# Kernel optimization log

Hardware: AMD Instinct MI355X
Metric: run time of the kernel (lower is better)

The kernel has to match this reference:

```python
import jax, jax.numpy as jnp
import numpy as np

B, S, H = 1, 2048, 1024
NH, NKV, HD = 16, 4, 64  # n_attn_heads, n_kv_heads, head_dim


def setup_inputs() -> dict:
    key = jax.random.key(0)
    k1, k2, k3, k4 = jax.random.split(key, 4)
    x = jax.random.normal(k1, (B, S, H), dtype=jnp.float32)
    Wq = jax.random.normal(k2, (H, H), dtype=jnp.float32) * 0.02
    Wk = jax.random.normal(k3, (NKV * HD, H), dtype=jnp.float32) * 0.02
    Wv = jax.random.normal(k4, (NKV * HD, H), dtype=jnp.float32) * 0.02
    return {"x": x, "Wq": Wq, "Wk": Wk, "Wv": Wv}


def reference(x, Wq, Wk, Wv):
    b, s, h = x.shape
    rep = NH // NKV
    # projections (torch Linear: x @ W.T)
    q = (x @ Wq.T).reshape(b, s, NH, HD).transpose(0, 2, 1, 3)      # [b, NH, s, d]
    k = (x @ Wk.T).reshape(b, s, NKV, HD).transpose(0, 2, 1, 3)     # [b, NKV, s, d]
    v = (x @ Wv.T).reshape(b, s, NKV, HD).transpose(0, 2, 1, 3)
    # repeat_kv: expand each kv head rep times
    k = jnp.repeat(k, rep, axis=1)                                   # [b, NH, s, d]
    v = jnp.repeat(v, rep, axis=1)
    # NOTE: source scales by 1/sqrt(hidden_size), not 1/sqrt(head_dim)
    scale = 1.0 / np.sqrt(H).astype(np.float32)
    scores = jnp.einsum('bhqd,bhkd->bhqk', q, k) * scale             # [b, NH, s, s]
    causal = jnp.tril(jnp.ones((s, s), dtype=bool))
    scores = jnp.where(causal[None, None], scores, -jnp.inf)
    probs = jax.nn.softmax(scores, axis=-1)
    y = jnp.einsum('bhqk,bhkd->bhqd', probs, v)                      # [b, NH, s, d]
    return y.transpose(0, 2, 1, 3).reshape(b, s, NH * HD)
```

## Files before the change

kernel.cpp:

```cpp
#include <hip/hip_runtime.h>

#define S_LEN 2048
#define HID   1024
#define NHEAD 16
#define NKVH  4
#define HDIM  64
#define NPROJ 1536
#define QKSTR 1280

typedef __bf16 bf16x8 __attribute__((ext_vector_type(8)));
typedef float  f32x4  __attribute__((ext_vector_type(4)));

typedef const __attribute__((address_space(1))) void* gas_ptr;
typedef __attribute__((address_space(3))) void*       las_ptr;

#define QSCALE 0.04508422f

__device__ __forceinline__ unsigned short f2bf(float f) {
    unsigned u = __builtin_bit_cast(unsigned, f);
    u = u + 0x7FFFu + ((u >> 16) & 1u);
    return (unsigned short)(u >> 16);
}

__global__ __launch_bounds__(256) void cvt_all(
    const float* __restrict__ x,  const float* __restrict__ wq,
    const float* __restrict__ wk, const float* __restrict__ wv,
    unsigned short* __restrict__ xbf, unsigned short* __restrict__ wbf)
{
    const long nx  = (long)S_LEN * HID;
    const long nwq = (long)HID * HID;
    const long nwk = (long)256 * HID;
    long i = (long)(blockIdx.x * 256 + threadIdx.x) * 4;
    const float* src; unsigned short* dst;
    if (i < nx)                  { src = x  + i;                 dst = xbf + i; }
    else if (i < nx + nwq)       { long j = i - nx;              src = wq + j; dst = wbf + j; }
    else if (i < nx + nwq + nwk) { long j = i - nx - nwq;        src = wk + j; dst = wbf + nwq + j; }
    else                         { long j = i - nx - nwq - nwk;  src = wv + j; dst = wbf + nwq + nwk + j; }
    float4 v = *(const float4*)src;
    ushort4 o; o.x = f2bf(v.x); o.y = f2bf(v.y); o.z = f2bf(v.z); o.w = f2bf(v.w);
    *(ushort4*)dst = o;
}

__global__ __launch_bounds__(256) void proj_gemm(
    const unsigned short* __restrict__ xbf,
    const unsigned short* __restrict__ wbf,
    unsigned short* __restrict__ qkv,
    unsigned short* __restrict__ vT)
{
    __shared__ unsigned short At[2][128 * 64];
    __shared__ unsigned short Bt[2][96 * 64];
    const int tid = threadIdx.x;
    const int w = tid >> 6, l = tid & 63;
    const int quad = l >> 4, lane16 = l & 15;
    const int m0 = blockIdx.y * 128, n0 = blockIdx.x * 96;
    const int wm = (w & 1) * 64, wn = (w >> 1) * 48;

    const int srow = l >> 3;
    const int scol = ((l & 7) ^ srow) * 8;

    f32x4 acc[4][3] = {};

    #define STAGE(KT, BUF)                                                              \
        do {                                                                            \
            _Pragma("unroll")                                                           \
            for (int c = 0; c < 4; ++c) {                                               \
                const int rbase = w * 32 + c * 8;                                       \
                const unsigned short* ga =                                              \
                    xbf + (long)(m0 + rbase + srow) * HID + (KT) + scol;                \
                __builtin_amdgcn_global_load_lds((gas_ptr)ga,                           \
                    (las_ptr)&At[BUF][rbase * 64], 16, 0, 0);                           \
            }                                                                           \
            _Pragma("unroll")                                                           \
            for (int c = 0; c < 3; ++c) {                                               \
                const int rbase = w * 24 + c * 8;                                       \
                const unsigned short* gb =                                              \
                    wbf + (long)(n0 + rbase + srow) * HID + (KT) + scol;                \
                __builtin_amdgcn_global_load_lds((gas_ptr)gb,                           \
                    (las_ptr)&Bt[BUF][rbase * 64], 16, 0, 0);                           \
            }                                                                           \
        } while (0)

    STAGE(0, 0);

    for (int i = 0; i < 16; ++i) {
        const int cur = i & 1;
        __syncthreads();
        if (i + 1 < 16) STAGE((i + 1) * 64, cur ^ 1);

        #pragma unroll
        for (int ks = 0; ks < 2; ++ks) {
            const int swz = ((ks * 4 + quad) ^ (lane16 & 7)) * 8;
            bf16x8 a[4], b[3];
            #pragma unroll
            for (int mi = 0; mi < 4; ++mi)
                a[mi] = *(const bf16x8*)&At[cur][(wm + mi * 16 + lane16) * 64 + swz];
            #pragma unroll
            for (int ni = 0; ni < 3; ++ni)
                b[ni] = *(const bf16x8*)&Bt[cur][(wn + ni * 16 + lane16) * 64 + swz];
            #pragma unroll
            for (int mi = 0; mi < 4; ++mi)
                #pragma unroll
                for (int ni = 0; ni < 3; ++ni)
                    acc[mi][ni] = __builtin_amdgcn_mfma_f32_16x16x32_bf16(a[mi], b[ni], acc[mi][ni], 0, 0, 0);
        }
    }
    #undef STAGE

    #pragma unroll
    for (int mi = 0; mi < 4; ++mi) {
        const int row = m0 + wm + mi * 16 + quad * 4;
        #pragma unroll
        for (int ni = 0; ni < 3; ++ni) {
            const int col = n0 + wn + ni * 16 + lane16;
            #pragma unroll
            for (int r = 0; r < 4; ++r) {
                const float v = acc[mi][ni][r];
                if (col < 1024)
                    qkv[(long)(row + r) * QKSTR + col] = f2bf(v * QSCALE);
                else if (col < 1280)
                    qkv[(long)(row + r) * QKSTR + col] = f2bf(v);
                else
                    vT[(long)(col - 1280) * S_LEN + (row + r)] = f2bf(v);
            }
        }
    }
}

#define KSTR 72
__global__ __launch_bounds__(256) void attn(
    const unsigned short* __restrict__ qkv,
    const unsigned short* __restrict__ vT,
    float* __restrict__ out)
{
    __shared__ unsigned short Kt[2][64 * KSTR];
    __shared__ unsigned short Vt[2][64 * KSTR];
    __shared__ unsigned short Pb[4 * 16 * KSTR];

    const int tid = threadIdx.x;
    const int w = tid >> 6, l = tid & 63;
    const int quad = l >> 4, lane16 = l & 15;
    const int bx = blockIdx.x, by = blockIdx.y;
    const int qt = (by & 8) ? (31 - bx) : bx;
    const int h  = by;
    const int kh = h >> 2;
    const int qcol = h * 64;
    const int kcol = 1024 + kh * 64;

    const long qrow = (long)(qt * 64 + w * 16 + lane16);
    bf16x8 qa0 = *(const bf16x8*)&qkv[qrow * QKSTR + qcol + quad * 8];
    bf16x8 qa1 = *(const bf16x8*)&qkv[qrow * QKSTR + qcol + 32 + quad * 8];

    f32x4 o[4] = {};
    float rsum[4] = {0.f, 0.f, 0.f, 0.f};

    unsigned short* pw = &Pb[w * 16 * KSTR];

    const int sr = tid >> 2, ss = tid & 3;
    const long vrow = (long)(kh * 64 + sr) * S_LEN;

    bf16x8 kr0, kr1, vr0, vr1;
    {
        const long gk = (long)sr * QKSTR + kcol + ss * 16;
        kr0 = *(const bf16x8*)&qkv[gk];
        kr1 = *(const bf16x8*)&qkv[gk + 8];
        const long gv = vrow + ss * 16;
        vr0 = *(const bf16x8*)&vT[gv];
        vr1 = *(const bf16x8*)&vT[gv + 8];
    }

    for (int kt = 0; kt <= qt; ++kt) {
        const int cur = kt & 1;
        *(bf16x8*)&Kt[cur][sr * KSTR + ss * 16]     = kr0;
        *(bf16x8*)&Kt[cur][sr * KSTR + ss * 16 + 8] = kr1;
        *(bf16x8*)&Vt[cur][sr * KSTR + ss * 16]     = vr0;
        *(bf16x8*)&Vt[cur][sr * KSTR + ss * 16 + 8] = vr1;
        if (kt < qt) {
            const long gk = (long)((kt + 1) * 64 + sr) * QKSTR + kcol + ss * 16;
            kr0 = *(const bf16x8*)&qkv[gk];
            kr1 = *(const bf16x8*)&qkv[gk + 8];
            const long gv = vrow + (kt + 1) * 64 + ss * 16;
            vr0 = *(const bf16x8*)&vT[gv];
            vr1 = *(const bf16x8*)&vT[gv + 8];
        }
        __syncthreads();

        f32x4 sacc[4] = {};
        #pragma unroll
        for (int t = 0; t < 4; ++t) {
            bf16x8 kb0 = *(const bf16x8*)&Kt[cur][(t * 16 + lane16) * KSTR + quad * 8];
            bf16x8 kb1 = *(const bf16x8*)&Kt[cur][(t * 16 + lane16) * KSTR + 32 + quad * 8];
            sacc[t] = __builtin_amdgcn_mfma_f32_16x16x32_bf16(qa0, kb0, sacc[t], 0, 0, 0);
            sacc[t] = __builtin_amdgcn_mfma_f32_16x16x32_bf16(qa1, kb1, sacc[t], 0, 0, 0);
        }

        if (kt == qt) {
            #pragma unroll
            for (int t = 0; t < 4; ++t) {
                const int colw = t * 16 + lane16;
                #pragma unroll
                for (int r = 0; r < 4; ++r)
                    if (colw > w * 16 + quad * 4 + r) sacc[t][r] = -3.0e38f;
            }
        }

        #pragma unroll
        for (int t = 0; t < 4; ++t)
            #pragma unroll
            for (int r = 0; r < 4; ++r) {
                const float p = __builtin_amdgcn_exp2f(sacc[t][r]);
                rsum[r] += p;
                const int row = quad * 4 + r;
                const int col = t * 16 + lane16;
                pw[row * KSTR + (col ^ ((row & 12) << 1))] = f2bf(p);
            }


        #pragma unroll
        for (int ks = 0; ks < 2; ++ks) {
            bf16x8 pa = *(const bf16x8*)&pw[lane16 * KSTR + ((ks * 32 + quad * 8) ^ ((lane16 & 12) << 1))];
            #pragma unroll
            for (int t = 0; t < 4; ++t) {
                bf16x8 vb = *(const bf16x8*)&Vt[cur][(t * 16 + lane16) * KSTR + ks * 32 + quad * 8];
                o[t] = __builtin_amdgcn_mfma_f32_16x16x32_bf16(pa, vb, o[t], 0, 0, 0);
            }
        }
    }

    float inv[4];
    #pragma unroll
    for (int r = 0; r < 4; ++r) {
        float v = rsum[r];
        v += __shfl_xor(v, 1);
        v += __shfl_xor(v, 2);
        v += __shfl_xor(v, 4);
        v += __shfl_xor(v, 8);
        inv[r] = 1.0f / v;
    }
    const int orow = qt * 64 + w * 16 + quad * 4;
    #pragma unroll
    for (int t = 0; t < 4; ++t) {
        const int col = h * 64 + t * 16 + lane16;
        #pragma unroll
        for (int r = 0; r < 4; ++r)
            out[(long)(orow + r) * (NHEAD * HDIM) + col] = o[t][r] * inv[r];
    }
}

extern "C" void kernel_launch(void* const* d_in, const int* in_sizes, int n_in,
                              void* d_out, int out_size, void* d_ws, size_t ws_size,
                              hipStream_t stream) {
    const float* x  = (const float*)d_in[0];
    const float* wq = (const float*)d_in[1];
    const float* wk = (const float*)d_in[2];
    const float* wv = (const float*)d_in[3];
    float* out = (float*)d_out;

    unsigned short* xbf = (unsigned short*)d_ws;
    unsigned short* wbf = xbf + (size_t)S_LEN * HID;
    unsigned short* qkv = wbf + (size_t)NPROJ * HID;
    unsigned short* vT  = qkv + (size_t)S_LEN * QKSTR;

    cvt_all<<<dim3(3584), dim3(256), 0, stream>>>(x, wq, wk, wv, xbf, wbf);
    proj_gemm<<<dim3(16, 16), dim3(256), 0, stream>>>(xbf, wbf, qkv, vT);
    attn<<<dim3(32, 16), dim3(256), 0, stream>>>(qkv, vT, out);
}
```

Baseline: 124.1 us.

## Load K/V fragments directly from global into registers, drop shared staging

```diff
diff --git a/kernel.cpp b/kernel.cpp
--- a/kernel.cpp
+++ b/kernel.cpp
@@ -132,8 +132,6 @@
     const unsigned short* __restrict__ vT,
     float* __restrict__ out)
 {
-    __shared__ unsigned short Kt[2][64 * KSTR];
-    __shared__ unsigned short Vt[2][64 * KSTR];
     __shared__ unsigned short Pb[4 * 16 * KSTR];
 
     const int tid = threadIdx.x;
@@ -155,76 +153,74 @@
 
     unsigned short* pw = &Pb[w * 16 * KSTR];
 
-    const int sr = tid >> 2, ss = tid & 3;
-    const long vrow = (long)(kh * 64 + sr) * S_LEN;
-
-    bf16x8 kr0, kr1, vr0, vr1;
-    {
-        const long gk = (long)sr * QKSTR + kcol + ss * 16;
-        kr0 = *(const bf16x8*)&qkv[gk];
-        kr1 = *(const bf16x8*)&qkv[gk + 8];
-        const long gv = vrow + ss * 16;
-        vr0 = *(const bf16x8*)&vT[gv];
-        vr1 = *(const bf16x8*)&vT[gv + 8];
-    }
-
-    for (int kt = 0; kt <= qt; ++kt) {
-        const int cur = kt & 1;
-        *(bf16x8*)&Kt[cur][sr * KSTR + ss * 16]     = kr0;
-        *(bf16x8*)&Kt[cur][sr * KSTR + ss * 16 + 8] = kr1;
-        *(bf16x8*)&Vt[cur][sr * KSTR + ss * 16]     = vr0;
-        *(bf16x8*)&Vt[cur][sr * KSTR + ss * 16 + 8] = vr1;
-        if (kt < qt) {
-            const long gk = (long)((kt + 1) * 64 + sr) * QKSTR + kcol + ss * 16;
-            kr0 = *(const bf16x8*)&qkv[gk];
-            kr1 = *(const bf16x8*)&qkv[gk + 8];
-            const long gv = vrow + (kt + 1) * 64 + ss * 16;
-            vr0 = *(const bf16x8*)&vT[gv];
-            vr1 = *(const bf16x8*)&vT[gv + 8];
-        }
-        __syncthreads();
-
-        f32x4 sacc[4] = {};
-        #pragma unroll
-        for (int t = 0; t < 4; ++t) {
-            bf16x8 kb0 = *(const bf16x8*)&Kt[cur][(t * 16 + lane16) * KSTR + quad * 8];
-            bf16x8 kb1 = *(const bf16x8*)&Kt[cur][(t * 16 + lane16) * KSTR + 32 + quad * 8];
-            sacc[t] = __builtin_amdgcn_mfma_f32_16x16x32_bf16(qa0, kb0, sacc[t], 0, 0, 0);
-            sacc[t] = __builtin_amdgcn_mfma_f32_16x16x32_bf16(qa1, kb1, sacc[t], 0, 0, 0);
-        }
-
-        if (kt == qt) {
-            #pragma unroll
-            for (int t = 0; t < 4; ++t) {
-                const int colw = t * 16 + lane16;
-                #pragma unroll
-                for (int r = 0; r < 4; ++r)
-                    if (colw > w * 16 + quad * 4 + r) sacc[t][r] = -3.0e38f;
-            }
-        }
-
-        #pragma unroll
-        for (int t = 0; t < 4; ++t)
-            #pragma unroll
-            for (int r = 0; r < 4; ++r) {
-                const float p = __builtin_amdgcn_exp2f(sacc[t][r]);
-                rsum[r] += p;
-                const int row = quad * 4 + r;
-                const int col = t * 16 + lane16;
-                pw[row * KSTR + (col ^ ((row & 12) << 1))] = f2bf(p);
-            }
-
-
-        #pragma unroll
-        for (int ks = 0; ks < 2; ++ks) {
-            bf16x8 pa = *(const bf16x8*)&pw[lane16 * KSTR + ((ks * 32 + quad * 8) ^ ((lane16 & 12) << 1))];
-            #pragma unroll
-            for (int t = 0; t < 4; ++t) {
-                bf16x8 vb = *(const bf16x8*)&Vt[cur][(t * 16 + lane16) * KSTR + ks * 32 + quad * 8];
-                o[t] = __builtin_amdgcn_mfma_f32_16x16x32_bf16(pa, vb, o[t], 0, 0, 0);
-            }
-        }
-    }
+    #define LOADK(DST, KT)                                                            \
+        _Pragma("unroll")                                                             \
+        for (int t = 0; t < 4; ++t)                                                   \
+            _Pragma("unroll")                                                         \
+            for (int ks = 0; ks < 2; ++ks)                                            \
+                DST[t][ks] = *(const bf16x8*)&qkv[                                    \
+                    (long)((KT) * 64 + t * 16 + lane16) * QKSTR + kcol + ks * 32 + quad * 8];
+
+    #define LOADV(DST, KT)                                                            \
+        _Pragma("unroll")                                                             \
+        for (int t = 0; t < 4; ++t)                                                   \
+            _Pragma("unroll")                                                         \
+            for (int ks = 0; ks < 2; ++ks)                                            \
+                DST[t][ks] = *(const bf16x8*)&vT[                                     \
+                    (long)(kh * 64 + t * 16 + lane16) * S_LEN + (KT) * 64 + ks * 32 + quad * 8];
+
+    #define STEP(KB, KBN, KT)                                                         \
+    {                                                                                 \
+        bf16x8 vb[4][2];                                                              \
+        LOADV(vb, KT);                                      \
+        f32x4 sacc[4] = {};                                                           \
+        _Pragma("unroll")                                                             \
+        for (int t = 0; t < 4; ++t) {                                                 \
+            sacc[t] = __builtin_amdgcn_mfma_f32_16x16x32_bf16(qa0, KB[t][0], sacc[t], 0, 0, 0); \
+            sacc[t] = __builtin_amdgcn_mfma_f32_16x16x32_bf16(qa1, KB[t][1], sacc[t], 0, 0, 0); \
+        }                                                                             \
+        if ((KT) < qt) { LOADK(KBN, (KT) + 1); }              \
+        if ((KT) == qt) {                             \
+            _Pragma("unroll")                                                         \
+            for (int t = 0; t < 4; ++t) {                                             \
+                const int colw = t * 16 + lane16;                                     \
+                _Pragma("unroll")                                                     \
+                for (int r = 0; r < 4; ++r)                                           \
+                    if (colw > w * 16 + quad * 4 + r) sacc[t][r] = -3.0e38f;          \
+            }                                                                         \
+        }                                                                             \
+        _Pragma("unroll")                                                             \
+        for (int t = 0; t < 4; ++t)                                                   \
+            _Pragma("unroll")                                                         \
+            for (int r = 0; r < 4; ++r) {                                             \
+                const float p = __builtin_amdgcn_exp2f(sacc[t][r]);                   \
+                rsum[r] += p;                                                         \
+                const int row = quad * 4 + r;                                         \
+                const int col = t * 16 + lane16;                                      \
+                pw[row * KSTR + (col ^ ((row & 12) << 1))] = f2bf(p);                 \
+            }                                                                         \
+        _Pragma("unroll")                                                             \
+        for (int ks = 0; ks < 2; ++ks) {                                              \
+            bf16x8 pa = *(const bf16x8*)&pw[lane16 * KSTR +                           \
+                            ((ks * 32 + quad * 8) ^ ((lane16 & 12) << 1))];           \
+            _Pragma("unroll")                                                         \
+            for (int t = 0; t < 4; ++t)                                               \
+                o[t] = __builtin_amdgcn_mfma_f32_16x16x32_bf16(pa, vb[t][ks], o[t], 0, 0, 0); \
+        }                                                                             \
+    }
+
+    bf16x8 kba[4][2], kbb[4][2];
+    LOADK(kba, 0);
+    int kt = 0;
+    for (;;) {
+        STEP(kba, kbb, kt);
+        if (++kt > qt) break;
+        STEP(kbb, kba, kt);
+        if (++kt > qt) break;
+    }
+    #undef STEP
+    #undef LOADK
+    #undef LOADV
 
     float inv[4];
     #pragma unroll
```

After: 156.1 us. 25.8% more time.
